# Optimization experiments

Measured on AMD Instinct MI355X. Metric: run time of the kernel, lower is better.

## Reference

```python
import jax, jax.numpy as jnp
from jax import lax
import numpy as np

B, T = 64, 1024
N_MELS, ENC, DEC, LSTM, SPK = 80, 256, 128, 512, 256
CTX = ENC + SPK          # encoder_seq feature dim = 512
PRE = 2 * DEC            # prenet fc dims = 256
FILTERS, KS = 32, 31
MAX_R, R = 20, 1         # r buffer initialized to 1
DROP_P = 0.5


def _gru_cell(x, h, w_ih, w_hh, b_ih, b_hh):
    gi = x @ w_ih.T + b_ih
    gh = h @ w_hh.T + b_hh
    i_r, i_z, i_n = jnp.split(gi, 3, axis=-1)
    h_r, h_z, h_n = jnp.split(gh, 3, axis=-1)
    r = jax.nn.sigmoid(i_r + h_r)
    z = jax.nn.sigmoid(i_z + h_z)
    n = jnp.tanh(i_n + r * h_n)
    return (1.0 - z) * n + z * h


def _lstm_cell(x, h, c, w_ih, w_hh, b_ih, b_hh):
    g = x @ w_ih.T + h @ w_hh.T + b_ih + b_hh
    i, f, gg, o = jnp.split(g, 4, axis=-1)
    c2 = jax.nn.sigmoid(f) * c + jax.nn.sigmoid(i) * jnp.tanh(gg)
    h2 = jax.nn.sigmoid(o) * jnp.tanh(c2)
    return h2, c2


def setup_inputs() -> dict:
    key = jax.random.key(0)
    ks = jax.random.split(key, 40)
    n = lambda i, shp: jax.random.normal(ks[i], shp, jnp.float32)
    p = lambda i, shp: jax.random.normal(ks[i], shp, jnp.float32) * 0.05
    return {
        "encoder_seq": n(0, (B, T, CTX)),
        "encoder_seq_proj": n(1, (B, T, DEC)),
        "prenet_in": n(2, (B, N_MELS)),
        "attn_hidden": n(3, (B, DEC)),
        "rnn1_hidden": n(4, (B, LSTM)),
        "rnn2_hidden": n(5, (B, LSTM)),
        "rnn1_cell": n(6, (B, LSTM)),
        "rnn2_cell": n(7, (B, LSTM)),
        "context_vec": n(8, (B, CTX)),
        "chars": jax.random.randint(ks[9], (B, T), 0, 100),
        "t": 0,
        # LSA params (torch layout: Linear weight [out,in])
        "conv_w": p(10, (FILTERS, 1, KS)),
        "conv_b": p(11, (FILTERS,)),
        "L_w": p(12, (DEC, FILTERS)),
        "W_w": p(13, (DEC, DEC)),
        "W_b": p(14, (DEC,)),
        "v_w": p(15, (1, DEC)),
        # PreNet
        "fc1_w": p(16, (PRE, N_MELS)),
        "fc1_b": p(17, (PRE,)),
        "fc2_w": p(18, (PRE, PRE)),
        "fc2_b": p(19, (PRE,)),
        # GRUCell: in = CTX + PRE = 768, hidden = DEC
        "gru_w_ih": p(20, (3 * DEC, CTX + PRE)),
        "gru_w_hh": p(21, (3 * DEC, DEC)),
        "gru_b_ih": p(22, (3 * DEC,)),
        "gru_b_hh": p(23, (3 * DEC,)),
        # rnn_input Linear: CTX + DEC = 640 -> LSTM
        "ri_w": p(24, (LSTM, CTX + DEC)),
        "ri_b": p(25, (LSTM,)),
        # LSTMCells
        "l1_w_ih": p(26, (4 * LSTM, LSTM)),
        "l1_w_hh": p(27, (4 * LSTM, LSTM)),
        "l1_b_ih": p(28, (4 * LSTM,)),
        "l1_b_hh": p(29, (4 * LSTM,)),
        "l2_w_ih": p(30, (4 * LSTM, LSTM)),
        "l2_w_hh": p(31, (4 * LSTM, LSTM)),
        "l2_b_ih": p(32, (4 * LSTM,)),
        "l2_b_hh": p(33, (4 * LSTM,)),
        # output projections
        "mp_w": p(34, (N_MELS * MAX_R, LSTM)),
        "sp_w": p(35, (1, CTX + LSTM)),
        "sp_b": p(36, (1,)),
    }


def reference(encoder_seq, encoder_seq_proj, prenet_in, attn_hidden, rnn1_hidden,
              rnn2_hidden, rnn1_cell, rnn2_cell, context_vec, chars, t,
              conv_w, conv_b, L_w, W_w, W_b, v_w,
              fc1_w, fc1_b, fc2_w, fc2_b,
              gru_w_ih, gru_w_hh, gru_b_ih, gru_b_hh,
              ri_w, ri_b,
              l1_w_ih, l1_w_hh, l1_b_ih, l1_b_hh,
              l2_w_ih, l2_w_hh, l2_b_ih, l2_b_hh,
              mp_w, sp_w, sp_b):
    # PreNet (dropout always on, deterministic keys)
    dk1, dk2 = jax.random.split(jax.random.key(42))
    keep = 1.0 - DROP_P
    h = jax.nn.relu(prenet_in @ fc1_w.T + fc1_b)
    h = h * jax.random.bernoulli(dk1, keep, h.shape).astype(h.dtype) / keep
    h = jax.nn.relu(h @ fc2_w.T + fc2_b)
    prenet_out = h * jax.random.bernoulli(dk2, keep, h.shape).astype(h.dtype) / keep

    # attention GRU
    attn_h = _gru_cell(jnp.concatenate([context_vec, prenet_out], axis=-1),
                       attn_hidden, gru_w_ih, gru_w_hh, gru_b_ih, gru_b_hh)

    # LSA attention at t == 0 (cumulative attention is zeros)
    pq = attn_h @ W_w.T + W_b                              # [B, DEC]
    cumulative = jnp.zeros((B, 1, T), encoder_seq.dtype)
    loc = lax.conv_general_dilated(cumulative, conv_w, (1,), [((KS - 1) // 2,) * 2],
                                   dimension_numbers=("NCH", "OIH", "NCH"))
    loc = loc + conv_b[None, :, None]                      # [B, F, T]
    ploc = jnp.swapaxes(loc, 1, 2) @ L_w.T                 # [B, T, DEC]
    u = (jnp.tanh(pq[:, None, :] + encoder_seq_proj + ploc) @ v_w.T)[..., 0]  # [B, T]
    u = u * (chars != 0).astype(u.dtype)
    scores = jax.nn.softmax(u, axis=1)                     # [B, T]
    context = jnp.einsum("bt,btd->bd", scores, encoder_seq)  # [B, CTX]

    # residual LSTM stack (inference: no zoneout)
    x = jnp.concatenate([context, attn_h], axis=1) @ ri_w.T + ri_b
    h1, c1 = _lstm_cell(x, rnn1_hidden, rnn1_cell, l1_w_ih, l1_w_hh, l1_b_ih, l1_b_hh)
    x = x + h1
    h2, c2 = _lstm_cell(x, rnn2_hidden, rnn2_cell, l2_w_ih, l2_w_hh, l2_b_ih, l2_b_hh)
    x = x + h2

    mels = (x @ mp_w.T).reshape(B, N_MELS, MAX_R)[:, :, :R]  # [B, n_mels, r]
    stop = jax.nn.sigmoid(jnp.concatenate([x, context], axis=1) @ sp_w.T + sp_b)
    return mels, scores[:, None, :], attn_h, h1, h2, c1, c2, context, stop
```

## Files before the change

kernel.cpp:

```cpp
#include <hip/hip_runtime.h>
#include <stdint.h>

#define JAX_PARTITIONABLE 1
#define NB 1024

__device__ __forceinline__ float tanh_f(float x) {
  float e = __expf(2.0f * x);
  return 1.0f - 2.0f / (e + 1.0f);
}
__device__ __forceinline__ float sigm(float x) {
  return 1.0f / (1.0f + __expf(-x));
}

__device__ __forceinline__ void stw(float* p, float v) {
  __hip_atomic_store(p, v, __ATOMIC_RELAXED, __HIP_MEMORY_SCOPE_AGENT);
}
__device__ __forceinline__ void stw4(float* p, float4 v) {
  union { float2 f; uint64_t u; } a, b;
  a.f.x = v.x; a.f.y = v.y; b.f.x = v.z; b.f.y = v.w;
  __hip_atomic_store((uint64_t*)p, a.u, __ATOMIC_RELAXED, __HIP_MEMORY_SCOPE_AGENT);
  __hip_atomic_store(((uint64_t*)p) + 1, b.u, __ATOMIC_RELAXED, __HIP_MEMORY_SCOPE_AGENT);
}

__device__ __forceinline__ void tf2x32(unsigned k0, unsigned k1, unsigned x0, unsigned x1,
                                       unsigned &o0, unsigned &o1) {
  unsigned ks0 = k0, ks1 = k1, ks2 = k0 ^ k1 ^ 0x1BD11BDAu;
  x0 += ks0; x1 += ks1;
#define RR(r) { x0 += x1; x1 = (x1 << r) | (x1 >> (32 - r)); x1 ^= x0; }
  RR(13) RR(15) RR(26) RR(6)  x0 += ks1; x1 += ks2 + 1u;
  RR(17) RR(29) RR(16) RR(24) x0 += ks2; x1 += ks0 + 2u;
  RR(13) RR(15) RR(26) RR(6)  x0 += ks0; x1 += ks1 + 3u;
  RR(17) RR(29) RR(16) RR(24) x0 += ks1; x1 += ks2 + 4u;
  RR(13) RR(15) RR(26) RR(6)  x0 += ks2; x1 += ks0 + 5u;
#undef RR
  o0 = x0; o1 = x1;
}

__device__ __forceinline__ float drop_scale(unsigned k0, unsigned k1, unsigned flat) {
#if JAX_PARTITIONABLE
  unsigned o0, o1; tf2x32(k0, k1, 0u, flat, o0, o1);
  unsigned bits = o0 ^ o1;
#else
  unsigned o0, o1, bits;
  if (flat < 8192u) { tf2x32(k0, k1, flat, flat + 8192u, o0, o1); bits = o0; }
  else             { tf2x32(k0, k1, flat - 8192u, flat, o0, o1); bits = o1; }
#endif
  return (bits >> 31) ? 0.0f : 2.0f;
}
__device__ __forceinline__ void get_drop_keys(unsigned &a0, unsigned &a1,
                                              unsigned &b0, unsigned &b1) {
#if JAX_PARTITIONABLE
  tf2x32(0u, 42u, 0u, 0u, a0, a1);
  tf2x32(0u, 42u, 0u, 1u, b0, b1);
#else
  unsigned p0, q0, p1, q1;
  tf2x32(0u, 42u, 0u, 2u, p0, q0);
  tf2x32(0u, 42u, 1u, 3u, p1, q1);
  a0 = p0; a1 = p1; b0 = q0; b1 = q1;
#endif
}

__device__ __forceinline__ void gbar(int* ibase, int phase) {
  __syncthreads();
  if (threadIdx.x == 0) {
    const int s = (int)(blockIdx.x & 31);
    int* sub   = ibase + s * 64;
    int* top   = ibase + 2048;
    int* flags = ibase + 2112;
    int old = __hip_atomic_fetch_add(sub, 1, __ATOMIC_RELAXED, __HIP_MEMORY_SCOPE_AGENT);
    if (old == phase * 32 - 1) {
      int t = __hip_atomic_fetch_add(top, 1, __ATOMIC_RELAXED, __HIP_MEMORY_SCOPE_AGENT);
      if (t == phase * 32 - 1) {
        #pragma unroll
        for (int i = 0; i < 32; i++)
          __hip_atomic_store(flags + i * 64, phase, __ATOMIC_RELAXED, __HIP_MEMORY_SCOPE_AGENT);
      }
    }
    long long guard = 0;
    while (__hip_atomic_load(flags + s * 64, __ATOMIC_RELAXED, __HIP_MEMORY_SCOPE_AGENT) < phase) {
      __builtin_amdgcn_s_sleep(4);
      if (++guard > (1LL << 21)) break;
    }
  }
  __syncthreads();
}

__global__ void k0(int* cnt) {
  for (int i = threadIdx.x; i < 4160; i += 256) cnt[i] = 0;
}

__global__ __launch_bounds__(256, 4) void kM(
    const float* es, const float* esp, const float* prenet_in,
    const float* rnn1_hidden, const float* rnn2_hidden,
    const float* rnn1_cell, const float* rnn2_cell,
    const float* context_vec, const float* attn_hidden, const int* chars,
    const float* conv_b, const float* L_w, const float* W_w, const float* W_b, const float* v_w,
    const float* fc1_w, const float* fc1_b, const float* fc2_w, const float* fc2_b,
    const float* gru_w_ih, const float* gru_w_hh, const float* gru_b_ih, const float* gru_b_hh,
    const float* ri_w, const float* ri_b,
    const float* l1_w_ih, const float* l1_w_hh, const float* l1_b_ih, const float* l1_b_hh,
    const float* l2_w_ih, const float* l2_w_hh, const float* l2_b_ih, const float* l2_b_hh,
    const float* mp_w, const float* sp_w, const float* sp_b,
    float* ws,
    float* mels_o, float* scores_o, float* attn_o, float* h1_o, float* h2_o,
    float* c1_o, float* c2_o, float* ctx_o, float* stop_o) {
  int* ibase = (int*)ws;
  float* pqc    = ws + 4160;
  float* phq    = ws + 4288;
  float* poq    = ws + 20672;
  float* ahq_h  = ws + 37056;
  float* u_buf  = ws + 45248;
  float* ctxq   = ws + 110784;
  float* xq     = ws + 143552;
  float* x2q    = ws + 176320;
  float* x3q    = ws + 209088;
  float* hq1    = ws + 241856;
  float* hq2    = ws + 274624;
  float* cvq    = ws + 307392;
  float* ahq_in = ws + 340160;
  float* c1pT   = ws + 348352;
  float* c2pT   = ws + 381120;

  const float4* cvq4   = (const float4*)cvq;
  const float4* phq4   = (const float4*)phq;
  const float4* poq4   = (const float4*)poq;
  const float4* ahq_in4= (const float4*)ahq_in;
  const float4* ahq_h4 = (const float4*)ahq_h;
  const float4* ctxq4  = (const float4*)ctxq;
  const float4* xq4    = (const float4*)xq;
  const float4* x2q4   = (const float4*)x2q;
  const float4* x3q4   = (const float4*)x3q;
  const float4* hq14   = (const float4*)hq1;
  const float4* hq24   = (const float4*)hq2;

  const int g = blockIdx.x, tid = threadIdx.x;
  const int w = tid >> 6, lane = tid & 63;
  __shared__ float sh[5440];

  if (g < 64) {
    for (int i = tid; i < 5120; i += 256) sh[(i / 80) * 81 + (i % 80)] = prenet_in[i];
    __syncthreads();
    unsigned d1k0, d1k1, d2k0, d2k1;
    get_drop_keys(d1k0, d1k1, d2k0, d2k1);
    const int j = g * 4 + w;
    float acc = fc1_b[j];
    const float* wr = fc1_w + j * 80;
    #pragma unroll 8
    for (int k = 0; k < 80; k += 2) {
      float2 wv = *(const float2*)(wr + k);
      acc += sh[lane * 81 + k] * wv.x + sh[lane * 81 + k + 1] * wv.y;
    }
    acc = fmaxf(acc, 0.0f) * drop_scale(d1k0, d1k1, (unsigned)(lane * 256 + j));
    stw(&phq[g * 256 + lane * 4 + w], acc);
  } else if (g < 96) {
    int t = (g - 64) * 256 + tid;
    int k4 = t >> 6, b = t & 63;
    stw4(&hq1[k4 * 256 + b * 4], ((const float4*)rnn1_hidden)[b * 128 + k4]);
  } else if (g < 128) {
    int t = (g - 96) * 256 + tid;
    int k4 = t >> 6, b = t & 63;
    stw4(&hq2[k4 * 256 + b * 4], ((const float4*)rnn2_hidden)[b * 128 + k4]);
  } else if (g < 160) {
    int t = (g - 128) * 256 + tid;
    int k4 = t >> 6, b = t & 63;
    stw4(&cvq[k4 * 256 + b * 4], ((const float4*)context_vec)[b * 128 + k4]);
  } else if (g < 168) {
    int t = (g - 160) * 256 + tid;
    int k4 = t >> 6, b = t & 63;
    stw4(&ahq_in[k4 * 256 + b * 4], ((const float4*)attn_hidden)[b * 32 + k4]);
  } else if (g < 232) {
    int base = (g - 168) * 512;
    #pragma unroll
    for (int e = 0; e < 2; e++) { int i = base + tid + e * 256; stw(&c1pT[i], rnn1_cell[(i & 63) * 512 + (i >> 6)]); }
  } else if (g < 296) {
    int base = (g - 232) * 512;
    #pragma unroll
    for (int e = 0; e < 2; e++) { int i = base + tid + e * 256; stw(&c2pT[i], rnn2_cell[(i & 63) * 512 + (i >> 6)]); }
  } else if (g < 360) {
    int base = (g - 296) * 512;
    #pragma unroll
    for (int e = 0; e < 2; e++) stw(&ctxq[base + tid + e * 256], 0.0f);
  } else if (g == 360) {
    if (tid < 128) {
      float acc = W_b[tid];
      const float* lw = L_w + tid * 32;
      #pragma unroll
      for (int f = 0; f < 32; f++) acc += conv_b[f] * lw[f];
      stw(&pqc[tid], acc);
    }
  } else {
    const unsigned wi0 = (unsigned)((g - 361) * 256 + tid);
    float acc = 0.0f;
    #pragma unroll
    for (int s = 0; s < 4; s++) acc += es[(size_t)(wi0 + (unsigned)s * 169728u) * 32];
    asm volatile("" :: "v"(acc));
  }
  gbar(ibase, 1);

  if (g < 64) {
    const int j = g * 4 + w;
    ((float4*)(sh + w * 256))[lane] = ((const float4*)(fc2_w + j * 256))[lane];
    __syncthreads();
    unsigned d1k0, d1k1, d2k0, d2k1;
    get_drop_keys(d1k0, d1k1, d2k0, d2k1);
    const float4* wv4 = (const float4*)(sh + w * 256);
    float acc = fc2_b[j];
    #pragma unroll 8
    for (int k4 = 0; k4 < 64; k4++) {
      float4 x4 = phq4[k4 * 64 + lane];
      float4 wv = wv4[k4];
      acc += x4.x * wv.x + x4.y * wv.y + x4.z * wv.z + x4.w * wv.w;
    }
    acc = fmaxf(acc, 0.0f) * drop_scale(d2k0, d2k1, (unsigned)(lane * 256 + j));
    stw(&poq[g * 256 + lane * 4 + w], acc);
  } else {
    const unsigned wid = (unsigned)((g - 64) * 256 + tid);
    float acc = 0.0f;
    acc += esp[(size_t)wid * 32];
    if (wid < 16384u) acc += esp[(size_t)(wid + 245760u) * 32];
    if (wid < 32768u) {
      acc += l1_w_ih[(size_t)wid * 32];
      acc += l1_w_hh[(size_t)wid * 32];
      acc += l2_w_ih[(size_t)wid * 32];
      acc += l2_w_hh[(size_t)wid * 32];
    }
    if (wid < 10240u) acc += ri_w[(size_t)wid * 32];
    if (wid < 9216u)  acc += gru_w_ih[(size_t)wid * 32];
    if (wid < 1536u)  acc += gru_w_hh[(size_t)wid * 32];
    if (wid < 512u)   acc += W_w[(size_t)wid * 32];
    if (wid < 2048u)  acc += (float)chars[(size_t)wid * 32];
    if (wid < 1280u)  acc += mp_w[(size_t)(wid >> 4) * 10240 + (wid & 15) * 32];
    if (wid < 32u)    acc += sp_w[(size_t)wid * 32];
    asm volatile("" :: "v"(acc));
  }
  gbar(ibase, 2);

  if (g < 128) {
    if (w < 3) {
      const int rj = g + 128 * w;
      const float4* src = (const float4*)(gru_w_ih + (size_t)rj * 768);
      float4* dst = (float4*)(sh + w * 768);
      #pragma unroll
      for (int q = 0; q < 3; q++) dst[q * 64 + lane] = src[q * 64 + lane];
    } else {
      float4* dst = (float4*)(sh + 2304);
      if (lane < 32) {
        dst[lane]      = ((const float4*)gru_w_hh)[(size_t)g * 32 + lane];
        dst[32 + lane] = ((const float4*)gru_w_hh)[(size_t)(128 + g) * 32 + lane];
        dst[64 + lane] = ((const float4*)gru_w_hh)[(size_t)(256 + g) * 32 + lane];
      }
    }
    __syncthreads();
    if (w < 3) {
      const int rj = g + 128 * w;
      const float4* wv4 = (const float4*)(sh + w * 768);
      float acc = gru_b_ih[rj];
      #pragma unroll 4
      for (int k4 = 0; k4 < 128; k4++) {
        float4 x4 = cvq4[k4 * 64 + lane];
        float4 wv = wv4[k4];
        acc += x4.x * wv.x + x4.y * wv.y + x4.z * wv.z + x4.w * wv.w;
      }
      #pragma unroll 4
      for (int k4 = 0; k4 < 64; k4++) {
        float4 x4 = poq4[k4 * 64 + lane];
        float4 wv = wv4[128 + k4];
        acc += x4.x * wv.x + x4.y * wv.y + x4.z * wv.z + x4.w * wv.w;
      }
      sh[2688 + w * 64 + lane] = acc;
    } else {
      const float4* wh4 = (const float4*)(sh + 2304);
      #pragma unroll
      for (int r = 0; r < 3; r++) {
        float acc = gru_b_hh[r * 128 + g];
        #pragma unroll 4
        for (int k4 = 0; k4 < 32; k4++) {
          float4 x4 = ahq_in4[k4 * 64 + lane];
          float4 wv = wh4[r * 32 + k4];
          acc += x4.x * wv.x + x4.y * wv.y + x4.z * wv.z + x4.w * wv.w;
        }
        sh[2688 + (3 + r) * 64 + lane] = acc;
      }
    }
    __syncthreads();
    if (tid < 64) {
      float gr = sh[2688 + tid]       + sh[2688 + 192 + tid];
      float gz = sh[2688 + 64 + tid]  + sh[2688 + 256 + tid];
      float gin = sh[2688 + 128 + tid];
      float ghn = sh[2688 + 320 + tid];
      float a0 = ahq_in[(g >> 2) * 256 + tid * 4 + (g & 3)];
      float r = sigm(gr), z = sigm(gz);
      float h = (1.0f - z) * tanh_f(gin + r * ghn) + z * a0;
      stw(&ahq_h[(g >> 2) * 256 + tid * 4 + (g & 3)], h);
      attn_o[tid * 128 + g] = h;
    }
  } else {
    const unsigned wid = (unsigned)((g - 128) * 256 + tid);
    float acc = 0.0f;
    acc += es[(size_t)(678912u + wid) * 32];
    if (wid < 140288u) acc += es[(size_t)(908288u + wid) * 32];
    asm volatile("" :: "v"(acc));
  }
  gbar(ibase, 3);

  {
    const int b = g >> 4, tch = g & 15;
    float* shh = sh;
    float* pqs = sh + 128;
    if (tid < 128) shh[tid] = ahq_h[(tid >> 2) * 256 + b * 4 + (tid & 3)];
    __syncthreads();
    if (tid < 128) {
      const int n = tid;
      float acc = pqc[n];
      const float4* wr = (const float4*)(W_w + n * 128);
      #pragma unroll 8
      for (int k4 = 0; k4 < 32; k4++) {
        float4 wv = wr[k4];
        acc += shh[k4 * 4] * wv.x + shh[k4 * 4 + 1] * wv.y + shh[k4 * 4 + 2] * wv.z + shh[k4 * 4 + 3] * wv.w;
      }
      pqs[n] = acc;
    }
    __syncthreads();
    float2 p = *(const float2*)(pqs + 2 * lane);
    float2 v2 = *(const float2*)(v_w + 2 * lane);
    const int tb = tch * 64 + w * 16;
    const float* erow = esp + ((size_t)b * 1024 + tb) * 128 + 2 * lane;
    for (int i2 = 0; i2 < 4; i2++) {
      const float* er = erow + (size_t)i2 * 512;
      float2 e0 = *(const float2*)(er);
      float2 e1 = *(const float2*)(er + 128);
      float2 e2 = *(const float2*)(er + 256);
      float2 e3 = *(const float2*)(er + 384);
      float s0 = v2.x * tanh_f(p.x + e0.x) + v2.y * tanh_f(p.y + e0.y);
      float s1 = v2.x * tanh_f(p.x + e1.x) + v2.y * tanh_f(p.y + e1.y);
      float s2 = v2.x * tanh_f(p.x + e2.x) + v2.y * tanh_f(p.y + e2.y);
      float s3 = v2.x * tanh_f(p.x + e3.x) + v2.y * tanh_f(p.y + e3.y);
      for (int off = 32; off > 0; off >>= 1) {
        s0 += __shfl_down(s0, off, 64);
        s1 += __shfl_down(s1, off, 64);
        s2 += __shfl_down(s2, off, 64);
        s3 += __shfl_down(s3, off, 64);
      }
      if (lane == 0) {
        int t = tb + i2 * 4;
        stw(&u_buf[b * 1024 + t],     (chars[b * 1024 + t]     != 0) ? s0 : 0.0f);
        stw(&u_buf[b * 1024 + t + 1], (chars[b * 1024 + t + 1] != 0) ? s1 : 0.0f);
        stw(&u_buf[b * 1024 + t + 2], (chars[b * 1024 + t + 2] != 0) ? s2 : 0.0f);
        stw(&u_buf[b * 1024 + t + 3], (chars[b * 1024 + t + 3] != 0) ? s3 : 0.0f);
      }
    }
  }
  gbar(ibase, 4);

  {
    const int b = g >> 4, tch = g & 15;
    float* redm = sh;
    float* sc   = sh + 256;
    float* red4 = sh + 320;
    float4 uv = *(const float4*)(u_buf + b * 1024 + tid * 4);
    float m = fmaxf(fmaxf(uv.x, uv.y), fmaxf(uv.z, uv.w));
    redm[tid] = m;
    __syncthreads();
    for (int s = 128; s > 0; s >>= 1) { if (tid < s) redm[tid] = fmaxf(redm[tid], redm[tid + s]); __syncthreads(); }
    float M = redm[0];
    __syncthreads();
    float e0 = __expf(uv.x - M), e1 = __expf(uv.y - M), e2 = __expf(uv.z - M), e3 = __expf(uv.w - M);
    redm[tid] = e0 + e1 + e2 + e3;
    __syncthreads();
    for (int s = 128; s > 0; s >>= 1) { if (tid < s) redm[tid] += redm[tid + s]; __syncthreads(); }
    float inv = 1.0f / redm[0];
    if (tch == 0) {
      float4 r; r.x = e0 * inv; r.y = e1 * inv; r.z = e2 * inv; r.w = e3 * inv;
      *(float4*)(scores_o + b * 1024 + tid * 4) = r;
    }
    if (tid < 64) sc[tid] = __expf(u_buf[b * 1024 + tch * 64 + tid] - M) * inv;
    __syncthreads();
    float acc0 = 0, acc1 = 0, acc2 = 0, acc3 = 0, acc4 = 0, acc5 = 0, acc6 = 0, acc7 = 0;
    const float* base = es + ((size_t)b * 1024 + tch * 64) * 512 + lane * 8;
    for (int i = 0; i < 16; i += 2) {
      int t1 = 4 * i + w, t2 = t1 + 4;
      float4 wa1 = *(const float4*)(base + (size_t)t1 * 512);
      float4 wb1 = *(const float4*)(base + (size_t)t1 * 512 + 4);
      float4 wa2 = *(const float4*)(base + (size_t)t2 * 512);
      float4 wb2 = *(const float4*)(base + (size_t)t2 * 512 + 4);
      float s1 = sc[t1], s2 = sc[t2];
      acc0 += s1 * wa1.x + s2 * wa2.x; acc1 += s1 * wa1.y + s2 * wa2.y;
      acc2 += s1 * wa1.z + s2 * wa2.z; acc3 += s1 * wa1.w + s2 * wa2.w;
      acc4 += s1 * wb1.x + s2 * wb2.x; acc5 += s1 * wb1.y + s2 * wb2.y;
      acc6 += s1 * wb1.z + s2 * wb2.z; acc7 += s1 * wb1.w + s2 * wb2.w;
    }
    float* rr = red4 + w * 512 + lane * 8;
    rr[0] = acc0; rr[1] = acc1; rr[2] = acc2; rr[3] = acc3;
    rr[4] = acc4; rr[5] = acc5; rr[6] = acc6; rr[7] = acc7;
    __syncthreads();
    int d0 = tid * 2;
    float r0 = red4[d0] + red4[512 + d0] + red4[1024 + d0] + red4[1536 + d0];
    float r1 = red4[d0 + 1] + red4[512 + d0 + 1] + red4[1024 + d0 + 1] + red4[1536 + d0 + 1];
    atomicAdd(&ctxq[(d0 >> 2) * 256 + b * 4 + (d0 & 3)], r0);
    atomicAdd(&ctxq[((d0 + 1) >> 2) * 256 + b * 4 + ((d0 + 1) & 3)], r1);
  }
  gbar(ibase, 5);

  if (g < 512) {
    const int n = g;
    if (tid < 160) ((float4*)sh)[tid] = ((const float4*)(ri_w + (size_t)n * 640))[tid];
    if (tid < 64) ctx_o[tid * 512 + n] = ctxq[(n >> 2) * 256 + tid * 4 + (n & 3)];
    __syncthreads();
    float acc = 0.0f;
    for (int k4 = w * 40; k4 < w * 40 + 40; k4++) {
      float4 wv = ((float4*)sh)[k4];
      float4 x4 = (k4 < 128) ? ctxq4[k4 * 64 + lane] : ahq_h4[(k4 - 128) * 64 + lane];
      acc += x4.x * wv.x + x4.y * wv.y + x4.z * wv.z + x4.w * wv.w;
    }
    sh[640 + w * 64 + lane] = acc;
    __syncthreads();
    if (tid < 64) stw(&xq[(n >> 2) * 256 + tid * 4 + (n & 3)],
                      ri_b[n] + sh[640 + tid] + sh[704 + tid] + sh[768 + tid] + sh[832 + tid]);
  }
  gbar(ibase, 6);

  if (g < 512) {
    const int n = g + (w << 9);
    {
      const float4* si = (const float4*)(l1_w_ih + (size_t)n * 512);
      const float4* sh4 = (const float4*)(l1_w_hh + (size_t)n * 512);
      float4* di = (float4*)sh + w * 256;
      float4* dh = di + 128;
      #pragma unroll
      for (int q = 0; q < 2; q++) { di[q * 64 + lane] = si[q * 64 + lane]; dh[q * 64 + lane] = sh4[q * 64 + lane]; }
    }
    __syncthreads();
    const float4* di = (const float4*)sh + w * 256;
    const float4* dh = di + 128;
    float acc = l1_b_ih[n] + l1_b_hh[n];
    #pragma unroll 4
    for (int k4 = 0; k4 < 128; k4++) {
      float4 x4 = xq4[k4 * 64 + lane];
      float4 wv = di[k4];
      acc += x4.x * wv.x + x4.y * wv.y + x4.z * wv.z + x4.w * wv.w;
    }
    #pragma unroll 4
    for (int k4 = 0; k4 < 128; k4++) {
      float4 x4 = hq14[k4 * 64 + lane];
      float4 wv = dh[k4];
      acc += x4.x * wv.x + x4.y * wv.y + x4.z * wv.z + x4.w * wv.w;
    }
    sh[4096 + w * 64 + lane] = acc;
    __syncthreads();
    if (tid < 64) {
      float gi = sh[4096 + tid], gf = sh[4160 + tid], gg = sh[4224 + tid], go = sh[4288 + tid];
      float c = c1pT[g * 64 + tid];
      float c2 = sigm(gf) * c + sigm(gi) * tanh_f(gg);
      float h2v = sigm(go) * tanh_f(c2);
      h1_o[tid * 512 + g] = h2v;
      c1_o[tid * 512 + g] = c2;
      stw(&x2q[(g >> 2) * 256 + tid * 4 + (g & 3)],
          xq[(g >> 2) * 256 + tid * 4 + (g & 3)] + h2v);
    }
  }
  gbar(ibase, 7);

  if (g < 512) {
    const int n = g + (w << 9);
    {
      const float4* si = (const float4*)(l2_w_ih + (size_t)n * 512);
      const float4* sh4 = (const float4*)(l2_w_hh + (size_t)n * 512);
      float4* di = (float4*)sh + w * 256;
      float4* dh = di + 128;
      #pragma unroll
      for (int q = 0; q < 2; q++) { di[q * 64 + lane] = si[q * 64 + lane]; dh[q * 64 + lane] = sh4[q * 64 + lane]; }
    }
    __syncthreads();
    const float4* di = (const float4*)sh + w * 256;
    const float4* dh = di + 128;
    float acc = l2_b_ih[n] + l2_b_hh[n];
    #pragma unroll 4
    for (int k4 = 0; k4 < 128; k4++) {
      float4 x4 = x2q4[k4 * 64 + lane];
      float4 wv = di[k4];
      acc += x4.x * wv.x + x4.y * wv.y + x4.z * wv.z + x4.w * wv.w;
    }
    #pragma unroll 4
    for (int k4 = 0; k4 < 128; k4++) {
      float4 x4 = hq24[k4 * 64 + lane];
      float4 wv = dh[k4];
      acc += x4.x * wv.x + x4.y * wv.y + x4.z * wv.z + x4.w * wv.w;
    }
    sh[4096 + w * 64 + lane] = acc;
    __syncthreads();
    if (tid < 64) {
      float gi = sh[4096 + tid], gf = sh[4160 + tid], gg = sh[4224 + tid], go = sh[4288 + tid];
      float c = c2pT[g * 64 + tid];
      float c2 = sigm(gf) * c + sigm(gi) * tanh_f(gg);
      float h2v = sigm(go) * tanh_f(c2);
      h2_o[tid * 512 + g] = h2v;
      c2_o[tid * 512 + g] = c2;
      stw(&x3q[(g >> 2) * 256 + tid * 4 + (g & 3)],
          x2q[(g >> 2) * 256 + tid * 4 + (g & 3)] + h2v);
    }
  }
  gbar(ibase, 8);

  if (g < 80) {
    const int m = g;
    if (tid < 128) ((float4*)sh)[tid] = ((const float4*)(mp_w + (size_t)m * 20 * 512))[tid];
    __syncthreads();
    float acc = 0.0f;
    for (int k4 = w * 32; k4 < w * 32 + 32; k4++) {
      float4 x4 = x3q4[k4 * 64 + lane];
      float4 wv = ((float4*)sh)[k4];
      acc += x4.x * wv.x + x4.y * wv.y + x4.z * wv.z + x4.w * wv.w;
    }
    sh[512 + w * 64 + lane] = acc;
    __syncthreads();
    if (tid < 64) mels_o[tid * 80 + m] = sh[512 + tid] + sh[576 + tid] + sh[640 + tid] + sh[704 + tid];
  } else if (g == 80) {
    ((float4*)sh)[tid] = ((const float4*)sp_w)[tid];
    __syncthreads();
    float acc = 0.0f;
    for (int k4 = w * 32; k4 < w * 32 + 32; k4++) {
      float4 x4 = x3q4[k4 * 64 + lane];
      float4 c4 = ctxq4[k4 * 64 + lane];
      float4 w1 = ((float4*)sh)[k4];
      float4 w2 = ((float4*)sh)[128 + k4];
      acc += x4.x * w1.x + x4.y * w1.y + x4.z * w1.z + x4.w * w1.w;
      acc += c4.x * w2.x + c4.y * w2.y + c4.z * w2.z + c4.w * w2.w;
    }
    sh[1024 + w * 64 + lane] = acc;
    __syncthreads();
    if (tid < 64) stop_o[tid] = sigm(sp_b[0] + sh[1024 + tid] + sh[1088 + tid] + sh[1152 + tid] + sh[1216 + tid]);
  }
}

extern "C" void kernel_launch(void* const* d_in, const int* in_sizes, int n_in,
                              void* d_out, int out_size, void* d_ws, size_t ws_size,
                              hipStream_t stream) {
  const float* es          = (const float*)d_in[0];
  const float* esp         = (const float*)d_in[1];
  const float* prenet_in   = (const float*)d_in[2];
  const float* attn_hidden = (const float*)d_in[3];
  const float* rnn1_hidden = (const float*)d_in[4];
  const float* rnn2_hidden = (const float*)d_in[5];
  const float* rnn1_cell   = (const float*)d_in[6];
  const float* rnn2_cell   = (const float*)d_in[7];
  const float* context_vec = (const float*)d_in[8];
  const int* chars         = (const int*)d_in[9];
  const float* conv_b = (const float*)d_in[12];
  const float* L_w    = (const float*)d_in[13];
  const float* W_w    = (const float*)d_in[14];
  const float* W_b    = (const float*)d_in[15];
  const float* v_w    = (const float*)d_in[16];
  const float* fc1_w  = (const float*)d_in[17];
  const float* fc1_b  = (const float*)d_in[18];
  const float* fc2_w  = (const float*)d_in[19];
  const float* fc2_b  = (const float*)d_in[20];
  const float* gru_w_ih = (const float*)d_in[21];
  const float* gru_w_hh = (const float*)d_in[22];
  const float* gru_b_ih = (const float*)d_in[23];
  const float* gru_b_hh = (const float*)d_in[24];
  const float* ri_w   = (const float*)d_in[25];
  const float* ri_b   = (const float*)d_in[26];
  const float* l1_w_ih = (const float*)d_in[27];
  const float* l1_w_hh = (const float*)d_in[28];
  const float* l1_b_ih = (const float*)d_in[29];
  const float* l1_b_hh = (const float*)d_in[30];
  const float* l2_w_ih = (const float*)d_in[31];
  const float* l2_w_hh = (const float*)d_in[32];
  const float* l2_b_ih = (const float*)d_in[33];
  const float* l2_b_hh = (const float*)d_in[34];
  const float* mp_w = (const float*)d_in[35];
  const float* sp_w = (const float*)d_in[36];
  const float* sp_b = (const float*)d_in[37];

  float* out = (float*)d_out;
  float* ws = (float*)d_ws;

  float* mels_o   = out + 0;
  float* scores_o = out + 5120;
  float* attn_o   = out + 70656;
  float* h1_o     = out + 78848;
  float* h2_o     = out + 111616;
  float* c1_o     = out + 144384;
  float* c2_o     = out + 177152;
  float* ctx_o    = out + 209920;
  float* stop_o   = out + 242688;

  k0<<<1, 256, 0, stream>>>((int*)ws);
  kM<<<NB, 256, 0, stream>>>(es, esp, prenet_in, rnn1_hidden, rnn2_hidden,
                             rnn1_cell, rnn2_cell, context_vec, attn_hidden, chars,
                             conv_b, L_w, W_w, W_b, v_w,
                             fc1_w, fc1_b, fc2_w, fc2_b,
                             gru_w_ih, gru_w_hh, gru_b_ih, gru_b_hh,
                             ri_w, ri_b,
                             l1_w_ih, l1_w_hh, l1_b_ih, l1_b_hh,
                             l2_w_ih, l2_w_hh, l2_b_ih, l2_b_hh,
                             mp_w, sp_w, sp_b,
                             ws,
                             mels_o, scores_o, attn_o, h1_o, h2_o,
                             c1_o, c2_o, ctx_o, stop_o);
}
```

Baseline: 432.7 us.

## Replace hierarchical grid barrier with centralized flag barrier; drop encoder prefetch touches

The grid barrier changes from a two-level atomic counter tree to per-block arrival flags. Block 0 polls all the flags in parallel and then writes 32 release flags that the other blocks spin on. This is meant to cut atomic contention and serial fetch-add latency at each phase boundary. The change also removes the dummy strided loads that prefetched encoder_seq and encoder_seq_proj into cache during early phases. Later phases may therefore hit colder cache on those large tensors, and block 0 now does extra polling work.

New measurement: 411.6 us. 1.05x faster.

```diff
diff --git a/kernel.cpp b/kernel.cpp
--- a/kernel.cpp
+++ b/kernel.cpp
@@ -62,23 +62,35 @@
 
 __device__ __forceinline__ void gbar(int* ibase, int phase) {
   __syncthreads();
-  if (threadIdx.x == 0) {
-    const int s = (int)(blockIdx.x & 31);
-    int* sub   = ibase + s * 64;
-    int* top   = ibase + 2048;
-    int* flags = ibase + 2112;
-    int old = __hip_atomic_fetch_add(sub, 1, __ATOMIC_RELAXED, __HIP_MEMORY_SCOPE_AGENT);
-    if (old == phase * 32 - 1) {
-      int t = __hip_atomic_fetch_add(top, 1, __ATOMIC_RELAXED, __HIP_MEMORY_SCOPE_AGENT);
-      if (t == phase * 32 - 1) {
-        #pragma unroll
-        for (int i = 0; i < 32; i++)
-          __hip_atomic_store(flags + i * 64, phase, __ATOMIC_RELAXED, __HIP_MEMORY_SCOPE_AGENT);
-      }
-    }
+  int* arrival = ibase;
+  int* release = ibase + 1024;
+  if (threadIdx.x == 0)
+    __hip_atomic_store(arrival + blockIdx.x, phase, __ATOMIC_RELAXED, __HIP_MEMORY_SCOPE_AGENT);
+  if (blockIdx.x == 0) {
+    __shared__ int notdone;
+    const int t4 = threadIdx.x * 4;
     long long guard = 0;
-    while (__hip_atomic_load(flags + s * 64, __ATOMIC_RELAXED, __HIP_MEMORY_SCOPE_AGENT) < phase) {
-      __builtin_amdgcn_s_sleep(4);
+    for (;;) {
+      int a0 = __hip_atomic_load(arrival + t4 + 0, __ATOMIC_RELAXED, __HIP_MEMORY_SCOPE_AGENT);
+      int a1 = __hip_atomic_load(arrival + t4 + 1, __ATOMIC_RELAXED, __HIP_MEMORY_SCOPE_AGENT);
+      int a2 = __hip_atomic_load(arrival + t4 + 2, __ATOMIC_RELAXED, __HIP_MEMORY_SCOPE_AGENT);
+      int a3 = __hip_atomic_load(arrival + t4 + 3, __ATOMIC_RELAXED, __HIP_MEMORY_SCOPE_AGENT);
+      bool ok = (a0 >= phase) && (a1 >= phase) && (a2 >= phase) && (a3 >= phase);
+      if (threadIdx.x == 0) notdone = 0;
+      __syncthreads();
+      if (!ok) notdone = 1;
+      __syncthreads();
+      if (!notdone) break;
+      if (++guard > (1LL << 19)) break;
+      __builtin_amdgcn_s_sleep(2);
+    }
+    if (threadIdx.x < 32)
+      __hip_atomic_store(release + threadIdx.x * 64, phase, __ATOMIC_RELAXED, __HIP_MEMORY_SCOPE_AGENT);
+  } else if (threadIdx.x == 0) {
+    int* myrel = release + (int)(blockIdx.x & 31) * 64;
+    long long guard = 0;
+    while (__hip_atomic_load(myrel, __ATOMIC_RELAXED, __HIP_MEMORY_SCOPE_AGENT) < phase) {
+      __builtin_amdgcn_s_sleep(2);
       if (++guard > (1LL << 21)) break;
     }
   }
@@ -86,7 +98,7 @@
 }
 
 __global__ void k0(int* cnt) {
-  for (int i = threadIdx.x; i < 4160; i += 256) cnt[i] = 0;
+  for (int i = threadIdx.x; i < 3072; i += 256) cnt[i] = 0;
 }
 
 __global__ __launch_bounds__(256, 4) void kM(
@@ -188,12 +200,6 @@
       for (int f = 0; f < 32; f++) acc += conv_b[f] * lw[f];
       stw(&pqc[tid], acc);
     }
-  } else {
-    const unsigned wi0 = (unsigned)((g - 361) * 256 + tid);
-    float acc = 0.0f;
-    #pragma unroll
-    for (int s = 0; s < 4; s++) acc += es[(size_t)(wi0 + (unsigned)s * 169728u) * 32];
-    asm volatile("" :: "v"(acc));
   }
   gbar(ibase, 1);
 
@@ -216,8 +222,6 @@
   } else {
     const unsigned wid = (unsigned)((g - 64) * 256 + tid);
     float acc = 0.0f;
-    acc += esp[(size_t)wid * 32];
-    if (wid < 16384u) acc += esp[(size_t)(wid + 245760u) * 32];
     if (wid < 32768u) {
       acc += l1_w_ih[(size_t)wid * 32];
       acc += l1_w_hh[(size_t)wid * 32];
@@ -294,12 +298,6 @@
       stw(&ahq_h[(g >> 2) * 256 + tid * 4 + (g & 3)], h);
       attn_o[tid * 128 + g] = h;
     }
-  } else {
-    const unsigned wid = (unsigned)((g - 128) * 256 + tid);
-    float acc = 0.0f;
-    acc += es[(size_t)(678912u + wid) * 32];
-    if (wid < 140288u) acc += es[(size_t)(908288u + wid) * 32];
-    asm volatile("" :: "v"(acc));
   }
   gbar(ibase, 3);
 
```
